# Performance work log

Hardware: AMD Instinct MI355X
Metric: run time of the kernel (lower is better)

## Reference

```python
import jax, jax.numpy as jnp
import numpy as np

N_NODES = 100000
N_EDGES = 1600000
N_FEAT = 128
HIDDEN = 128
N_GRAPHS = 64
N_CLASSES = 10
BN_EPS = 1e-5


def setup_inputs() -> dict:
    key = jax.random.key(0)
    ks = jax.random.split(key, 24)
    glorot = lambda k, o, i: jax.random.normal(k, (o, i), jnp.float32) * (1.0 / np.sqrt(i))
    inp = {
        'x': jax.random.normal(ks[0], (N_NODES, N_FEAT), jnp.float32),
        'edge_index': jax.random.randint(ks[1], (2, N_EDGES), 0, N_NODES, jnp.int64),
        'batch': jnp.sort(jax.random.randint(ks[2], (N_NODES,), 0, N_GRAPHS, jnp.int64)),
        # GCNConv(128 -> 128)
        'gcn_w': glorot(ks[3], HIDDEN, N_FEAT),
        'gcn_b': jnp.zeros((HIDDEN,), jnp.float32),
        # SAGEConv layers 1, 2: lin_l (aggregated, with bias) + lin_r (root, no bias)
        'sage1_wl': glorot(ks[4], HIDDEN, HIDDEN),
        'sage1_bl': jnp.zeros((HIDDEN,), jnp.float32),
        'sage1_wr': glorot(ks[5], HIDDEN, HIDDEN),
        'sage2_wl': glorot(ks[6], HIDDEN, HIDDEN),
        'sage2_bl': jnp.zeros((HIDDEN,), jnp.float32),
        'sage2_wr': glorot(ks[7], HIDDEN, HIDDEN),
        # ClassifierBase: 128 -> 200 -> 100 -> 50 -> 10
        'clf_w0': glorot(ks[8], 200, HIDDEN), 'clf_b0': jnp.zeros((200,), jnp.float32),
        'clf_w1': glorot(ks[9], 100, 200), 'clf_b1': jnp.zeros((100,), jnp.float32),
        'clf_w2': glorot(ks[10], 50, 100), 'clf_b2': jnp.zeros((50,), jnp.float32),
        'clf_w3': glorot(ks[11], N_CLASSES, 50), 'clf_b3': jnp.zeros((N_CLASSES,), jnp.float32),
        # BatchNorm1d (eval mode, running_mean=0, running_var=1)
        'bn0_g': jnp.ones((200,), jnp.float32), 'bn0_b': jnp.zeros((200,), jnp.float32),
        'bn1_g': jnp.ones((100,), jnp.float32), 'bn1_b': jnp.zeros((100,), jnp.float32),
        'bn2_g': jnp.ones((50,), jnp.float32), 'bn2_b': jnp.zeros((50,), jnp.float32),
    }
    return inp


def _gcn_conv(x, src, dst, W, b):
    # PyG GCNConv: add self loops, symmetric deg^{-1/2} normalization
    xw = x @ W.T                                                  # [N, H]
    ones = jnp.ones(src.shape[0], xw.dtype)
    deg = jax.ops.segment_sum(ones, dst, num_segments=N_NODES) + 1.0  # self loops
    dinv = jax.lax.rsqrt(deg)
    norm = dinv[src] * dinv[dst]                                  # [E]
    out = jax.ops.segment_sum(xw[src] * norm[:, None], dst, num_segments=N_NODES)
    out = out + xw * (dinv * dinv)[:, None]                       # self-loop term deg^{-1}
    return out + b


def _sage_conv(x, src, dst, Wl, bl, Wr):
    # PyG SAGEConv (mean aggr): lin_l(mean_{j->i} x_j) + lin_r(x_i)
    ones = jnp.ones(src.shape[0], x.dtype)
    cnt = jax.ops.segment_sum(ones, dst, num_segments=N_NODES)
    agg = jax.ops.segment_sum(x[src], dst, num_segments=N_NODES)
    agg = agg / jnp.maximum(cnt, 1.0)[:, None]
    return agg @ Wl.T + bl + x @ Wr.T


def _bn_eval(h, g, b):
    # eval-mode BatchNorm1d with running_mean=0, running_var=1
    return h * (g / np.sqrt(1.0 + BN_EPS)) + b


def reference(x, edge_index, batch, gcn_w, gcn_b,
              sage1_wl, sage1_bl, sage1_wr, sage2_wl, sage2_bl, sage2_wr,
              clf_w0, clf_b0, clf_w1, clf_b1, clf_w2, clf_b2, clf_w3, clf_b3,
              bn0_g, bn0_b, bn1_g, bn1_b, bn2_g, bn2_b):
    src, dst = edge_index[0], edge_index[1]
    h = _gcn_conv(x, src, dst, gcn_w, gcn_b)          # act_func is None -> no activation
    h = _sage_conv(h, src, dst, sage1_wl, sage1_bl, sage1_wr)
    h = _sage_conv(h, src, dst, sage2_wl, sage2_bl, sage2_wr)
    # global mean pool over graphs
    gcnt = jax.ops.segment_sum(jnp.ones(h.shape[0], h.dtype), batch, num_segments=N_GRAPHS)
    g = jax.ops.segment_sum(h, batch, num_segments=N_GRAPHS) / jnp.maximum(gcnt, 1.0)[:, None]
    # ClassifierBase (eval: dropout inactive), tanh activation
    g = jnp.tanh(_bn_eval(g @ clf_w0.T + clf_b0, bn0_g, bn0_b))
    g = jnp.tanh(_bn_eval(g @ clf_w1.T + clf_b1, bn1_g, bn1_b))
    g = jnp.tanh(_bn_eval(g @ clf_w2.T + clf_b2, bn2_g, bn2_b))
    logits = g @ clf_w3.T + clf_b3
    return jax.nn.softmax(logits, axis=1)             # [B, n_classes]
```

## Files before the change

kernel.cpp:

```cpp
#include <hip/hip_runtime.h>

#define N_NODES 100000
#define N_EDGES 1600000
#define NGRAPH 64
#define NBIN 391
#define EPB 6400
#define NBLK 250
#define CAPB 6144
#define CAP 8192
#define PSPLIT 8

typedef short s8v __attribute__((ext_vector_type(8)));
typedef float f4v __attribute__((ext_vector_type(4)));

__device__ __forceinline__ float bflo(unsigned u) { return __uint_as_float(u << 16); }
__device__ __forceinline__ float bfhi(unsigned u) { return __uint_as_float(u & 0xffff0000u); }
__device__ __forceinline__ unsigned short f2bf(float f) {
    unsigned u = __float_as_uint(f);
    u += 0x7fffu + ((u >> 16) & 1u);
    return (unsigned short)(u >> 16);
}
__device__ __forceinline__ float bf2f(unsigned short h) { return __uint_as_float(((unsigned)h) << 16); }
__device__ __forceinline__ unsigned pk(float lo, float hi) {
    return (unsigned)f2bf(lo) | ((unsigned)f2bf(hi) << 16);
}
__device__ __forceinline__ float ldv(const void* p, int i, int f32) {
    return f32 ? ((const float*)p)[i] : bf2f(((const unsigned short*)p)[i]);
}

__global__ __launch_bounds__(256) void k_setup(const unsigned short* __restrict__ x,
                                               const int* __restrict__ ei,
                                               const int* __restrict__ batch,
                                               int* __restrict__ flags,
                                               int* __restrict__ binCur,
                                               int* __restrict__ gstart,
                                               float* __restrict__ pbuf,
                                               const void* b0, const void* bn0g, const void* bn0b,
                                               const void* b1, const void* bn1g, const void* bn1b,
                                               const void* b2, const void* bn2g, const void* bn2b,
                                               const void* b3) {
    __shared__ int cnt[3];
    int tid = threadIdx.x;
    if (tid < 3) cnt[tid] = 0;
    __syncthreads();
    unsigned short h = x[tid * 37];
    int e = (h >> 7) & 0xFF;
    if (e >= 100 && e <= 150) atomicAdd(&cnt[0], 1);
    if (ei[2 * (tid * 5000) + 1] == 0) atomicAdd(&cnt[1], 1);
    if (batch[2 * (tid * 193) + 1] == 0) atomicAdd(&cnt[2], 1);
    __syncthreads();
    int f = (cnt[0] == 256) ? 0 : 1;
    int b64 = (cnt[2] == 256) ? 1 : 0;
    if (tid == 0) {
        flags[0] = f;
        flags[1] = (cnt[1] == 256) ? 1 : 0;
        flags[2] = b64;
    }
    for (int i = tid; i < NBIN; i += 256) binCur[i] = i * CAPB;
    if (tid <= NGRAPH) {
        int g = tid, lo = 0, hi = N_NODES;
        while (lo < hi) {
            int mid = (lo + hi) >> 1;
            int v = b64 ? batch[2 * mid] : batch[mid];
            if (v < g) lo = mid + 1;
            else hi = mid;
        }
        gstart[g] = lo;
    }
    const float invs = rsqrtf(1.0f + 1e-5f);
    if (tid < 200) {
        float a = ldv(bn0g, tid, f) * invs;
        pbuf[tid] = a;
        pbuf[200 + tid] = ldv(b0, tid, f) * a + ldv(bn0b, tid, f);
    }
    if (tid < 100) {
        float a = ldv(bn1g, tid, f) * invs;
        pbuf[400 + tid] = a;
        pbuf[500 + tid] = ldv(b1, tid, f) * a + ldv(bn1b, tid, f);
    }
    if (tid < 50) {
        float a = ldv(bn2g, tid, f) * invs;
        pbuf[600 + tid] = a;
        pbuf[650 + tid] = ldv(b2, tid, f) * a + ldv(bn2b, tid, f);
    }
    if (tid < 10) pbuf[700 + tid] = ldv(b3, tid, f);
}

__global__ __launch_bounds__(256) void k_binfill(const int* __restrict__ ei,
                                                 int* __restrict__ binCur,
                                                 unsigned* __restrict__ staging,
                                                 const int* __restrict__ flags) {
    __shared__ int cnt[NBIN];
    __shared__ int lofs[NBIN];
    __shared__ int curL[NBIN];
    __shared__ int basg[NBIN];
    __shared__ int sA[512], sB[512];
    __shared__ unsigned ebuf[EPB];
    int tid = threadIdx.x;
    int i64 = flags[1];
    int base = blockIdx.x * EPB;
    for (int i = tid; i < NBIN; i += 256) cnt[i] = 0;
    __syncthreads();
    for (int k = 0; k < EPB / 256; ++k) {
        int e = base + k * 256 + tid;
        int d = i64 ? ei[2 * (N_EDGES + e)] : ei[N_EDGES + e];
        if ((unsigned)d < N_NODES) atomicAdd(&cnt[d >> 8], 1);
    }
    __syncthreads();
    for (int k = tid; k < 512; k += 256) sA[k] = (k < NBIN) ? cnt[k] : 0;
    __syncthreads();
    int* src = sA;
    int* dst = sB;
    for (int off = 1; off < 512; off <<= 1) {
        for (int k = tid; k < 512; k += 256)
            dst[k] = src[k] + ((k >= off) ? src[k - off] : 0);
        __syncthreads();
        int* t = src; src = dst; dst = t;
    }
    for (int i = tid; i < NBIN; i += 256) {
        int excl = src[i] - cnt[i];
        lofs[i] = excl;
        curL[i] = excl;
        basg[i] = cnt[i] ? atomicAdd(&binCur[i], cnt[i]) : 0;
    }
    __syncthreads();
    for (int k = 0; k < EPB / 256; ++k) {
        int e = base + k * 256 + tid;
        int s = i64 ? ei[2 * e] : ei[e];
        int d = i64 ? ei[2 * (N_EDGES + e)] : ei[N_EDGES + e];
        if ((unsigned)d < N_NODES) {
            s = min(max(s, 0), N_NODES - 1);
            int p = atomicAdd(&curL[d >> 8], 1);
            ebuf[p] = ((unsigned)(d & 255) << 20) | (unsigned)s;
        }
    }
    __syncthreads();
    int wid = tid >> 6, lane = tid & 63;
    for (int b = wid; b < NBIN; b += 4) {
        int n = cnt[b], lo = lofs[b], go = basg[b];
        int cap = (b + 1) * CAPB;
        for (int l = lane; l < n; l += 64)
            if (go + l < cap) staging[go + l] = ebuf[lo + l];
    }
}

__global__ __launch_bounds__(256) void k_csr(const unsigned* __restrict__ staging,
                                             const int* __restrict__ binCur,
                                             int* __restrict__ rsA, int* __restrict__ reA,
                                             float* __restrict__ dinv,
                                             int* __restrict__ colidx) {
    __shared__ int deg[256];
    __shared__ int s[256];
    __shared__ int cur[256];
    __shared__ unsigned ebuf[CAP];
    __shared__ int colbuf[CAP];
    int b = blockIdx.x, tid = threadIdx.x;
    int n0 = b << 8;
    int nend = min(256, N_NODES - n0);
    int runStart = b * CAPB;
    int runLen = min(binCur[b] - runStart, CAPB);
    deg[tid] = 0;
    __syncthreads();
    for (int i = tid; i < runLen; i += 256) {
        unsigned e = staging[runStart + i];
        ebuf[i] = e;
        atomicAdd(&deg[e >> 20], 1);
    }
    __syncthreads();
    int myDeg = deg[tid];
    s[tid] = myDeg;
    __syncthreads();
    for (int off = 1; off < 256; off <<= 1) {
        int x2 = (tid >= off) ? s[tid - off] : 0;
        __syncthreads();
        s[tid] += x2;
        __syncthreads();
    }
    int incl = s[tid];
    if (tid < nend) {
        rsA[n0 + tid] = runStart + incl - myDeg;
        reA[n0 + tid] = runStart + incl;
        dinv[n0 + tid] = rsqrtf((float)myDeg + 1.0f);
    }
    cur[tid] = incl - myDeg;
    __syncthreads();
    for (int i = tid; i < runLen; i += 256) {
        unsigned e = ebuf[i];
        int p = atomicAdd(&cur[e >> 20], 1);
        colbuf[p] = (int)(e & 0xFFFFF);
    }
    __syncthreads();
    for (int i = tid; i < runLen; i += 256) colidx[runStart + i] = colbuf[i];
}

__global__ __launch_bounds__(256) void k_prescale(const void* __restrict__ src,
                                                  const float* __restrict__ dinv,
                                                  unsigned* __restrict__ out,
                                                  const int* __restrict__ flags) {
    int id = blockIdx.x * 256 + threadIdx.x;
    int node = id >> 6;
    float di = dinv[node];
    float lo, hi;
    if (flags[0]) {
        float2 u = ((const float2*)src)[id];
        lo = u.x; hi = u.y;
    } else {
        unsigned u = ((const unsigned*)src)[id];
        lo = bflo(u); hi = bfhi(u);
    }
    out[id] = pk(di * lo, di * hi);
}

__global__ __launch_bounds__(256) void k_agg(const uint4* __restrict__ xs,
                                             const int* __restrict__ rsA,
                                             const int* __restrict__ reA,
                                             const float* __restrict__ dinv,
                                             unsigned* __restrict__ out, int mode,
                                             const int* __restrict__ col) {
    int lane = threadIdx.x & 63;
    int node = blockIdx.x * 4 + (threadIdx.x >> 6);
    int glane = lane & 15, grp = lane >> 4;
    int rs = rsA[node], re = reA[node];
    int deg = re - rs;
    float a[8];
    #pragma unroll
    for (int i = 0; i < 8; ++i) a[i] = 0.f;
    uint4 selfu = make_uint4(0u, 0u, 0u, 0u);
    if (mode == 0) selfu = xs[(size_t)node * 16 + glane];

    int efull = rs + (deg & ~15);
    for (int base = rs; base < efull; base += 16) {
        int j0 = col[base + grp * 4 + 0];
        int j1 = col[base + grp * 4 + 1];
        int j2 = col[base + grp * 4 + 2];
        int j3 = col[base + grp * 4 + 3];
        uint4 u0 = xs[(size_t)j0 * 16 + glane];
        uint4 u1 = xs[(size_t)j1 * 16 + glane];
        uint4 u2 = xs[(size_t)j2 * 16 + glane];
        uint4 u3 = xs[(size_t)j3 * 16 + glane];
        a[0] += bflo(u0.x) + bflo(u1.x) + bflo(u2.x) + bflo(u3.x);
        a[1] += bfhi(u0.x) + bfhi(u1.x) + bfhi(u2.x) + bfhi(u3.x);
        a[2] += bflo(u0.y) + bflo(u1.y) + bflo(u2.y) + bflo(u3.y);
        a[3] += bfhi(u0.y) + bfhi(u1.y) + bfhi(u2.y) + bfhi(u3.y);
        a[4] += bflo(u0.z) + bflo(u1.z) + bflo(u2.z) + bflo(u3.z);
        a[5] += bfhi(u0.z) + bfhi(u1.z) + bfhi(u2.z) + bfhi(u3.z);
        a[6] += bflo(u0.w) + bflo(u1.w) + bflo(u2.w) + bflo(u3.w);
        a[7] += bfhi(u0.w) + bfhi(u1.w) + bfhi(u2.w) + bfhi(u3.w);
    }
    if (efull < re) {
        int j[4];
        float w[4];
        #pragma unroll
        for (int k = 0; k < 4; ++k) {
            int ee = efull + grp * 4 + k;
            bool v = ee < re;
            j[k] = col[v ? ee : re - 1];
            w[k] = v ? 1.f : 0.f;
        }
        uint4 u0 = xs[(size_t)j[0] * 16 + glane];
        uint4 u1 = xs[(size_t)j[1] * 16 + glane];
        uint4 u2 = xs[(size_t)j[2] * 16 + glane];
        uint4 u3 = xs[(size_t)j[3] * 16 + glane];
        a[0] += w[0] * bflo(u0.x) + w[1] * bflo(u1.x) + w[2] * bflo(u2.x) + w[3] * bflo(u3.x);
        a[1] += w[0] * bfhi(u0.x) + w[1] * bfhi(u1.x) + w[2] * bfhi(u2.x) + w[3] * bfhi(u3.x);
        a[2] += w[0] * bflo(u0.y) + w[1] * bflo(u1.y) + w[2] * bflo(u2.y) + w[3] * bflo(u3.y);
        a[3] += w[0] * bfhi(u0.y) + w[1] * bfhi(u1.y) + w[2] * bfhi(u2.y) + w[3] * bfhi(u3.y);
        a[4] += w[0] * bflo(u0.z) + w[1] * bflo(u1.z) + w[2] * bflo(u2.z) + w[3] * bflo(u3.z);
        a[5] += w[0] * bfhi(u0.z) + w[1] * bfhi(u1.z) + w[2] * bfhi(u2.z) + w[3] * bfhi(u3.z);
        a[6] += w[0] * bflo(u0.w) + w[1] * bflo(u1.w) + w[2] * bflo(u2.w) + w[3] * bflo(u3.w);
        a[7] += w[0] * bfhi(u0.w) + w[1] * bfhi(u1.w) + w[2] * bfhi(u2.w) + w[3] * bfhi(u3.w);
    }
    #pragma unroll
    for (int i = 0; i < 8; ++i) {
        float v = a[i];
        v += __shfl_xor(v, 16, 64);
        v += __shfl_xor(v, 32, 64);
        a[i] = v;
    }
    if (mode == 0) {
        float di = dinv[node];
        a[0] = di * (a[0] + bflo(selfu.x)); a[1] = di * (a[1] + bfhi(selfu.x));
        a[2] = di * (a[2] + bflo(selfu.y)); a[3] = di * (a[3] + bfhi(selfu.y));
        a[4] = di * (a[4] + bflo(selfu.z)); a[5] = di * (a[5] + bfhi(selfu.z));
        a[6] = di * (a[6] + bflo(selfu.w)); a[7] = di * (a[7] + bfhi(selfu.w));
    } else {
        float s = 1.0f / fmaxf((float)deg, 1.0f);
        #pragma unroll
        for (int i = 0; i < 8; ++i) a[i] *= s;
    }
    if (grp == 0) {
        uint4 o;
        o.x = pk(a[0], a[1]); o.y = pk(a[2], a[3]);
        o.z = pk(a[4], a[5]); o.w = pk(a[6], a[7]);
        *(uint4*)(out + (size_t)node * 64 + glane * 4) = o;
    }
}

template <int DUAL>
__global__ __launch_bounds__(256) void k_gemm(const unsigned short* A0,
                                              const void* __restrict__ W0,
                                              const unsigned short* __restrict__ A1,
                                              const void* __restrict__ W1,
                                              const void* __restrict__ bias,
                                              unsigned short* out,
                                              const int* __restrict__ flags) {
    __shared__ __align__(16) unsigned short As[64][136];
    __shared__ __align__(16) unsigned short Ws[128][136];
    int f32 = flags[0];
    int tid = threadIdx.x;
    int lane = tid & 63;
    int rowbase = blockIdx.x * 64;
    int lr = lane & 15, q = lane >> 4;
    int m0 = (tid >> 6) * 16;

    f4v acc[8];
    #pragma unroll
    for (int t = 0; t < 8; ++t) acc[t] = (f4v){0.f, 0.f, 0.f, 0.f};

    #pragma unroll
    for (int p = 0; p < (DUAL ? 2 : 1); ++p) {
        const unsigned short* Ap = p ? A1 : A0;
        const void* Wp = p ? W1 : W0;
        if (p) __syncthreads();
        #pragma unroll
        for (int it = 0; it < 4; ++it) {
            int chunk = tid + it * 256;
            int r = chunk >> 4, c8 = (chunk & 15) * 8;
            int grow = rowbase + r;
            uint4 v = make_uint4(0u, 0u, 0u, 0u);
            if (grow < N_NODES) v = *(const uint4*)(Ap + (size_t)grow * 128 + c8);
            *(uint4*)&As[r][c8] = v;
        }
        if (!f32) {
            const unsigned short* Wf = (const unsigned short*)Wp;
            #pragma unroll
            for (int it = 0; it < 8; ++it) {
                int chunk = tid + it * 256;
                int r = chunk >> 4, c8 = (chunk & 15) * 8;
                *(uint4*)&Ws[r][c8] = *(const uint4*)(Wf + r * 128 + c8);
            }
        } else {
            const float* Wf = (const float*)Wp;
            #pragma unroll
            for (int it = 0; it < 16; ++it) {
                int chunk = tid + it * 256;
                int r = chunk >> 5, c4 = (chunk & 31) * 4;
                float4 v = *(const float4*)(Wf + r * 128 + c4);
                unsigned lo = (unsigned)f2bf(v.x) | ((unsigned)f2bf(v.y) << 16);
                unsigned hi = (unsigned)f2bf(v.z) | ((unsigned)f2bf(v.w) << 16);
                *(uint2*)&Ws[r][c4] = make_uint2(lo, hi);
            }
        }
        __syncthreads();
        #pragma unroll
        for (int k = 0; k < 4; ++k) {
            s8v a = *(const s8v*)&As[m0 + lr][k * 32 + q * 8];
            #pragma unroll
            for (int t = 0; t < 8; ++t) {
                s8v b = *(const s8v*)&Ws[t * 16 + lr][k * 32 + q * 8];
                acc[t] = __builtin_amdgcn_mfma_f32_16x16x32_bf16(a, b, acc[t], 0, 0, 0);
            }
        }
    }
    #pragma unroll
    for (int t = 0; t < 8; ++t) {
        int o = t * 16 + lr;
        float bv = ldv(bias, o, f32);
        #pragma unroll
        for (int j = 0; j < 4; ++j) {
            int m = rowbase + m0 + q * 4 + j;
            if (m < N_NODES) out[(size_t)m * 128 + o] = f2bf(acc[t][j] + bv);
        }
    }
}

__global__ __launch_bounds__(256) void k_pool2(const unsigned* __restrict__ h,
                                               const int* __restrict__ gstart,
                                               float* __restrict__ ppool) {
    __shared__ float part[4][128];
    int g = blockIdx.x / PSPLIT, sl = blockIdx.x % PSPLIT;
    int wave = threadIdx.x >> 6, lane = threadIdx.x & 63;
    int s0 = gstart[g], s1 = gstart[g + 1];
    int n = s1 - s0;
    int chunk = (n + PSPLIT - 1) / PSPLIT;
    int r0 = s0 + sl * chunk;
    int r1 = min(r0 + chunk, s1);
    float a0 = 0.f, a1 = 0.f;
    for (int r = r0 + wave; r < r1; r += 4) {
        unsigned u = h[(size_t)r * 64 + lane];
        a0 += bflo(u);
        a1 += bfhi(u);
    }
    part[wave][2 * lane] = a0;
    part[wave][2 * lane + 1] = a1;
    __syncthreads();
    int t = threadIdx.x;
    if (t < 128) {
        float s = part[0][t] + part[1][t] + part[2][t] + part[3][t];
        ppool[(size_t)blockIdx.x * 128 + t] = s;
    }
}

__global__ void k_cvt_w(const void* w0, const void* w1, const void* w2, const void* w3,
                        float* __restrict__ wbuf, const int* __restrict__ flags) {
    int f = flags[0];
    int i = blockIdx.x * 256 + threadIdx.x;
    if (i < 25600) wbuf[i] = ldv(w0, i, f);
    else if (i < 45600) wbuf[i] = ldv(w1, i - 25600, f);
    else if (i < 50600) wbuf[i] = ldv(w2, i - 45600, f);
    else if (i < 51100) wbuf[i] = ldv(w3, i - 50600, f);
}

__global__ __launch_bounds__(256) void k_clf0(const float* __restrict__ ppool,
                                              const int* __restrict__ gstart,
                                              const float* __restrict__ wbuf,
                                              const float* __restrict__ pbuf,
                                              float* __restrict__ h1) {
    __shared__ float g[128];
    int b = blockIdx.x, t = threadIdx.x;
    if (t < 128) {
        float s = 0.f;
        #pragma unroll
        for (int k = 0; k < PSPLIT; ++k) s += ppool[(size_t)(b * PSPLIT + k) * 128 + t];
        int cnt = gstart[b + 1] - gstart[b];
        g[t] = s / fmaxf((float)cnt, 1.0f);
    }
    __syncthreads();
    if (t < 200) {
        const float4* wr = (const float4*)(wbuf + t * 128);
        float s = 0.f;
        #pragma unroll
        for (int k = 0; k < 32; ++k) {
            float4 v = wr[k];
            s += v.x * g[4 * k] + v.y * g[4 * k + 1] + v.z * g[4 * k + 2] + v.w * g[4 * k + 3];
        }
        h1[b * 200 + t] = tanhf(s * pbuf[t] + pbuf[200 + t]);
    }
}

__global__ __launch_bounds__(128) void k_clf1(const float* __restrict__ h1,
                                              const float* __restrict__ wbuf,
                                              const float* __restrict__ pbuf,
                                              float* __restrict__ h2) {
    __shared__ float g[200];
    int b = blockIdx.x, t = threadIdx.x;
    for (int i = t; i < 200; i += 128) g[i] = h1[b * 200 + i];
    __syncthreads();
    if (t < 100) {
        const float4* wr = (const float4*)(wbuf + 25600 + t * 200);
        float s = 0.f;
        #pragma unroll
        for (int k = 0; k < 50; ++k) {
            float4 v = wr[k];
            s += v.x * g[4 * k] + v.y * g[4 * k + 1] + v.z * g[4 * k + 2] + v.w * g[4 * k + 3];
        }
        h2[b * 100 + t] = tanhf(s * pbuf[400 + t] + pbuf[500 + t]);
    }
}

__global__ __launch_bounds__(128) void k_clf2(const float* __restrict__ h2,
                                              const float* __restrict__ wbuf,
                                              const float* __restrict__ pbuf,
                                              float* __restrict__ h3) {
    __shared__ float g[100];
    int b = blockIdx.x, t = threadIdx.x;
    if (t < 100) g[t] = h2[b * 100 + t];
    __syncthreads();
    if (t < 50) {
        const float4* wr = (const float4*)(wbuf + 45600 + t * 100);
        float s = 0.f;
        #pragma unroll
        for (int k = 0; k < 25; ++k) {
            float4 v = wr[k];
            s += v.x * g[4 * k] + v.y * g[4 * k + 1] + v.z * g[4 * k + 2] + v.w * g[4 * k + 3];
        }
        h3[b * 50 + t] = tanhf(s * pbuf[600 + t] + pbuf[650 + t]);
    }
}

__global__ __launch_bounds__(64) void k_clf3(const float* __restrict__ h3,
                                             const float* __restrict__ wbuf,
                                             const float* __restrict__ pbuf,
                                             void* outv, const int* __restrict__ flags) {
    int b = threadIdx.x;
    int f = flags[0];
    const float* h = h3 + b * 50;
    float lg[10];
    float mx = -1e30f;
    #pragma unroll
    for (int c = 0; c < 10; ++c) {
        const float* wr = wbuf + 50600 + c * 50;
        float s = 0.f;
        for (int k = 0; k < 50; ++k) s += wr[k] * h[k];
        s += pbuf[700 + c];
        lg[c] = s;
        mx = fmaxf(mx, s);
    }
    float sum = 0.f;
    #pragma unroll
    for (int c = 0; c < 10; ++c) {
        lg[c] = __expf(lg[c] - mx);
        sum += lg[c];
    }
    float inv = 1.0f / sum;
    #pragma unroll
    for (int c = 0; c < 10; ++c) {
        float v = lg[c] * inv;
        if (f) ((float*)outv)[b * 10 + c] = v;
        else ((unsigned short*)outv)[b * 10 + c] = f2bf(v);
    }
}

extern "C" void kernel_launch(void* const* d_in, const int* in_sizes, int n_in,
                              void* d_out, int out_size, void* d_ws, size_t ws_size,
                              hipStream_t stream) {
    const unsigned short* x16 = (const unsigned short*)d_in[0];
    const int* ei = (const int*)d_in[1];
    const int* batch = (const int*)d_in[2];

    char* ws = (char*)d_ws;
    size_t off = 0;
    auto alloc = [&](size_t bytes) {
        size_t r = off;
        off = (off + bytes + 255) & ~(size_t)255;
        return r;
    };
    int* flags = (int*)(ws + alloc(256));
    int* rsA = (int*)(ws + alloc((size_t)N_NODES * 4));
    int* reA = (int*)(ws + alloc((size_t)N_NODES * 4));
    int* colidx = (int*)(ws + alloc((size_t)NBIN * CAPB * 4));
    float* dinv = (float*)(ws + alloc((size_t)N_NODES * 4));
    int* binCur = (int*)(ws + alloc(NBIN * 4));
    int* gstart = (int*)(ws + alloc((NGRAPH + 1) * 4));
    float* pbuf = (float*)(ws + alloc(710 * 4));
    float* ppool = (float*)(ws + alloc((size_t)NGRAPH * PSPLIT * 128 * 4));
    float* wbuf = (float*)(ws + alloc(51100 * 4));
    float* h1 = (float*)(ws + alloc(64 * 200 * 4));
    float* h2 = (float*)(ws + alloc(64 * 100 * 4));
    float* h3 = (float*)(ws + alloc(64 * 50 * 4));
    unsigned short* bufA = (unsigned short*)(ws + alloc((size_t)N_NODES * 128 * 2));
    unsigned short* bufB = (unsigned short*)(ws + alloc((size_t)N_NODES * 128 * 2));
    unsigned* staging = (unsigned*)bufA;

    k_setup<<<1, 256, 0, stream>>>(x16, ei, batch, flags, binCur, gstart, pbuf,
                                   d_in[12], d_in[19], d_in[20],
                                   d_in[14], d_in[21], d_in[22],
                                   d_in[16], d_in[23], d_in[24], d_in[18]);
    k_cvt_w<<<200, 256, 0, stream>>>(d_in[11], d_in[13], d_in[15], d_in[17], wbuf, flags);

    k_binfill<<<NBLK, 256, 0, stream>>>(ei, binCur, staging, flags);
    k_csr<<<NBIN, 256, 0, stream>>>(staging, binCur, rsA, reA, dinv, colidx);

    k_prescale<<<N_NODES * 64 / 256, 256, 0, stream>>>((const void*)x16, dinv,
                                                       (unsigned*)bufB, flags);
    k_agg<<<N_NODES / 4, 256, 0, stream>>>((const uint4*)bufB, rsA, reA, dinv,
                                           (unsigned*)bufA, 0, colidx);
    k_gemm<0><<<(N_NODES + 63) / 64, 256, 0, stream>>>(bufA, d_in[3], nullptr, nullptr, d_in[4],
                                                       bufA, flags);
    k_agg<<<N_NODES / 4, 256, 0, stream>>>((const uint4*)bufA, rsA, reA, dinv,
                                           (unsigned*)bufB, 1, colidx);
    k_gemm<1><<<(N_NODES + 63) / 64, 256, 0, stream>>>(bufB, d_in[5], bufA, d_in[7], d_in[6],
                                                       bufB, flags);
    k_agg<<<N_NODES / 4, 256, 0, stream>>>((const uint4*)bufB, rsA, reA, dinv,
                                           (unsigned*)bufA, 1, colidx);
    k_gemm<1><<<(N_NODES + 63) / 64, 256, 0, stream>>>(bufA, d_in[8], bufB, d_in[10], d_in[9],
                                                       bufA, flags);
    k_pool2<<<NGRAPH * PSPLIT, 256, 0, stream>>>((const unsigned*)bufA, gstart, ppool);
    k_clf0<<<NGRAPH, 256, 0, stream>>>(ppool, gstart, wbuf, pbuf, h1);
    k_clf1<<<NGRAPH, 128, 0, stream>>>(h1, wbuf, pbuf, h2);
    k_clf2<<<NGRAPH, 128, 0, stream>>>(h2, wbuf, pbuf, h3);
    k_clf3<<<1, 64, 0, stream>>>(h3, wbuf, pbuf, d_out, flags);
}
```

Measured before the change: 517.7 us.

## Pad CSR rows to 32, fuse prescale into CSR build, merge classifier kernels

```diff
diff --git a/kernel.cpp b/kernel.cpp
--- a/kernel.cpp
+++ b/kernel.cpp
@@ -4,14 +4,15 @@
 #define N_EDGES 1600000
 #define NGRAPH 64
 #define NBIN 391
-#define EPB 6400
-#define NBLK 250
+#define EPB 2560
+#define NBLK 625
 #define CAPB 6144
-#define CAP 8192
+#define CAPP 8960
 #define PSPLIT 8
 
 typedef short s8v __attribute__((ext_vector_type(8)));
 typedef float f4v __attribute__((ext_vector_type(4)));
+typedef float f2v __attribute__((ext_vector_type(2)));
 
 __device__ __forceinline__ float bflo(unsigned u) { return __uint_as_float(u << 16); }
 __device__ __forceinline__ float bfhi(unsigned u) { return __uint_as_float(u & 0xffff0000u); }
@@ -26,6 +27,9 @@
 }
 __device__ __forceinline__ float ldv(const void* p, int i, int f32) {
     return f32 ? ((const float*)p)[i] : bf2f(((const unsigned short*)p)[i]);
+}
+__device__ __forceinline__ f2v up2(unsigned u) {
+    f2v t; t.x = bflo(u); t.y = bfhi(u); return t;
 }
 
 __global__ __launch_bounds__(256) void k_setup(const unsigned short* __restrict__ x,
@@ -95,16 +99,28 @@
     __shared__ int curL[NBIN];
     __shared__ int basg[NBIN];
     __shared__ int sA[512], sB[512];
+    __shared__ int dbuf[EPB];
     __shared__ unsigned ebuf[EPB];
     int tid = threadIdx.x;
     int i64 = flags[1];
     int base = blockIdx.x * EPB;
     for (int i = tid; i < NBIN; i += 256) cnt[i] = 0;
     __syncthreads();
-    for (int k = 0; k < EPB / 256; ++k) {
-        int e = base + k * 256 + tid;
-        int d = i64 ? ei[2 * (N_EDGES + e)] : ei[N_EDGES + e];
-        if ((unsigned)d < N_NODES) atomicAdd(&cnt[d >> 8], 1);
+    #pragma unroll
+    for (int k = 0; k < EPB / 512; ++k) {
+        int e = base + k * 512 + tid * 2;
+        int d0, d1;
+        if (i64) {
+            uint4 v = *(const uint4*)(ei + 2 * (size_t)(N_EDGES + e));
+            d0 = (int)v.x; d1 = (int)v.z;
+        } else {
+            int2 v = *(const int2*)(ei + (size_t)N_EDGES + e);
+            d0 = v.x; d1 = v.y;
+        }
+        int l = k * 512 + tid * 2;
+        dbuf[l] = d0; dbuf[l + 1] = d1;
+        if ((unsigned)d0 < N_NODES) atomicAdd(&cnt[d0 >> 8], 1);
+        if ((unsigned)d1 < N_NODES) atomicAdd(&cnt[d1 >> 8], 1);
     }
     __syncthreads();
     for (int k = tid; k < 512; k += 256) sA[k] = (k < NBIN) ? cnt[k] : 0;
@@ -124,14 +140,27 @@
         basg[i] = cnt[i] ? atomicAdd(&binCur[i], cnt[i]) : 0;
     }
     __syncthreads();
-    for (int k = 0; k < EPB / 256; ++k) {
-        int e = base + k * 256 + tid;
-        int s = i64 ? ei[2 * e] : ei[e];
-        int d = i64 ? ei[2 * (N_EDGES + e)] : ei[N_EDGES + e];
-        if ((unsigned)d < N_NODES) {
-            s = min(max(s, 0), N_NODES - 1);
-            int p = atomicAdd(&curL[d >> 8], 1);
-            ebuf[p] = ((unsigned)(d & 255) << 20) | (unsigned)s;
+    #pragma unroll
+    for (int k = 0; k < EPB / 512; ++k) {
+        int e = base + k * 512 + tid * 2;
+        int s0, s1;
+        if (i64) {
+            uint4 v = *(const uint4*)(ei + 2 * (size_t)e);
+            s0 = (int)v.x; s1 = (int)v.z;
+        } else {
+            int2 v = *(const int2*)(ei + (size_t)e);
+            s0 = v.x; s1 = v.y;
+        }
+        int l = k * 512 + tid * 2;
+        #pragma unroll
+        for (int h = 0; h < 2; ++h) {
+            int d = dbuf[l + h];
+            int s = h ? s1 : s0;
+            if ((unsigned)d < N_NODES) {
+                s = min(max(s, 0), N_NODES - 1);
+                int p = atomicAdd(&curL[d >> 8], 1);
+                ebuf[p] = ((unsigned)(d & 255) << 20) | (unsigned)s;
+            }
         }
     }
     __syncthreads();
@@ -148,16 +177,22 @@
                                              const int* __restrict__ binCur,
                                              int* __restrict__ rsA, int* __restrict__ reA,
                                              float* __restrict__ dinv,
-                                             int* __restrict__ colidx) {
+                                             int* __restrict__ colidx,
+                                             const void* __restrict__ x,
+                                             const int* __restrict__ flags,
+                                             unsigned* __restrict__ yout,
+                                             unsigned* __restrict__ padA) {
     __shared__ int deg[256];
     __shared__ int s[256];
     __shared__ int cur[256];
-    __shared__ unsigned ebuf[CAP];
-    __shared__ int colbuf[CAP];
+    __shared__ float sdinv[256];
+    __shared__ unsigned ebuf[CAPB];
+    __shared__ int colbuf[CAPP];
     int b = blockIdx.x, tid = threadIdx.x;
     int n0 = b << 8;
     int nend = min(256, N_NODES - n0);
     int runStart = b * CAPB;
+    int outStart = b * CAPP;
     int runLen = min(binCur[b] - runStart, CAPB);
     deg[tid] = 0;
     __syncthreads();
@@ -166,9 +201,11 @@
         ebuf[i] = e;
         atomicAdd(&deg[e >> 20], 1);
     }
+    for (int i = tid; i < CAPP; i += 256) colbuf[i] = N_NODES;
     __syncthreads();
     int myDeg = deg[tid];
-    s[tid] = myDeg;
+    int pdeg = (myDeg + 31) & ~31;
+    s[tid] = pdeg;
     __syncthreads();
     for (int off = 1; off < 256; off <<= 1) {
         int x2 = (tid >= off) ? s[tid - off] : 0;
@@ -177,38 +214,43 @@
         __syncthreads();
     }
     int incl = s[tid];
+    int lrs = incl - pdeg;
     if (tid < nend) {
-        rsA[n0 + tid] = runStart + incl - myDeg;
-        reA[n0 + tid] = runStart + incl;
-        dinv[n0 + tid] = rsqrtf((float)myDeg + 1.0f);
-    }
-    cur[tid] = incl - myDeg;
+        rsA[n0 + tid] = outStart + lrs;
+        reA[n0 + tid] = outStart + lrs + myDeg;
+        float di = rsqrtf((float)myDeg + 1.0f);
+        dinv[n0 + tid] = di;
+        sdinv[tid] = di;
+    }
+    cur[tid] = lrs;
     __syncthreads();
     for (int i = tid; i < runLen; i += 256) {
         unsigned e = ebuf[i];
         int p = atomicAdd(&cur[e >> 20], 1);
-        colbuf[p] = (int)(e & 0xFFFFF);
-    }
-    __syncthreads();
-    for (int i = tid; i < runLen; i += 256) colidx[runStart + i] = colbuf[i];
-}
-
-__global__ __launch_bounds__(256) void k_prescale(const void* __restrict__ src,
-                                                  const float* __restrict__ dinv,
-                                                  unsigned* __restrict__ out,
-                                                  const int* __restrict__ flags) {
-    int id = blockIdx.x * 256 + threadIdx.x;
-    int node = id >> 6;
-    float di = dinv[node];
-    float lo, hi;
-    if (flags[0]) {
-        float2 u = ((const float2*)src)[id];
-        lo = u.x; hi = u.y;
-    } else {
-        unsigned u = ((const unsigned*)src)[id];
-        lo = bflo(u); hi = bfhi(u);
-    }
-    out[id] = pk(di * lo, di * hi);
+        if (p < CAPP) colbuf[p] = (int)(e & 0xFFFFF);
+    }
+    __syncthreads();
+    int ptot = min(s[255], CAPP);
+    for (int i = tid; i < ptot; i += 256) colidx[outStart + i] = colbuf[i];
+    int f32 = flags[0];
+    for (int i = tid; i < nend * 64; i += 256) {
+        int nd = i >> 6;
+        float di = sdinv[nd];
+        size_t gid = (size_t)n0 * 64 + i;
+        float lo, hi;
+        if (f32) {
+            float2 u = ((const float2*)x)[gid];
+            lo = u.x; hi = u.y;
+        } else {
+            unsigned u = ((const unsigned*)x)[gid];
+            lo = bflo(u); hi = bfhi(u);
+        }
+        yout[gid] = pk(di * lo, di * hi);
+    }
+    if (b == 0 && tid < 64) {
+        yout[(size_t)N_NODES * 64 + tid] = 0u;
+        padA[(size_t)N_NODES * 64 + tid] = 0u;
+    }
 }
 
 __global__ __launch_bounds__(256) void k_agg(const uint4* __restrict__ xs,
@@ -222,76 +264,54 @@
     int glane = lane & 15, grp = lane >> 4;
     int rs = rsA[node], re = reA[node];
     int deg = re - rs;
-    float a[8];
-    #pragma unroll
-    for (int i = 0; i < 8; ++i) a[i] = 0.f;
+    int pend = rs + ((deg + 31) & ~31);
+    f2v a0 = {0.f, 0.f}, a1 = {0.f, 0.f}, a2 = {0.f, 0.f}, a3 = {0.f, 0.f};
     uint4 selfu = make_uint4(0u, 0u, 0u, 0u);
-    if (mode == 0) selfu = xs[(size_t)node * 16 + glane];
-
-    int efull = rs + (deg & ~15);
-    for (int base = rs; base < efull; base += 16) {
-        int j0 = col[base + grp * 4 + 0];
-        int j1 = col[base + grp * 4 + 1];
-        int j2 = col[base + grp * 4 + 2];
-        int j3 = col[base + grp * 4 + 3];
-        uint4 u0 = xs[(size_t)j0 * 16 + glane];
-        uint4 u1 = xs[(size_t)j1 * 16 + glane];
-        uint4 u2 = xs[(size_t)j2 * 16 + glane];
-        uint4 u3 = xs[(size_t)j3 * 16 + glane];
-        a[0] += bflo(u0.x) + bflo(u1.x) + bflo(u2.x) + bflo(u3.x);
-        a[1] += bfhi(u0.x) + bfhi(u1.x) + bfhi(u2.x) + bfhi(u3.x);
-        a[2] += bflo(u0.y) + bflo(u1.y) + bflo(u2.y) + bflo(u3.y);
-        a[3] += bfhi(u0.y) + bfhi(u1.y) + bfhi(u2.y) + bfhi(u3.y);
-        a[4] += bflo(u0.z) + bflo(u1.z) + bflo(u2.z) + bflo(u3.z);
-        a[5] += bfhi(u0.z) + bfhi(u1.z) + bfhi(u2.z) + bfhi(u3.z);
-        a[6] += bflo(u0.w) + bflo(u1.w) + bflo(u2.w) + bflo(u3.w);
-        a[7] += bfhi(u0.w) + bfhi(u1.w) + bfhi(u2.w) + bfhi(u3.w);
-    }
-    if (efull < re) {
-        int j[4];
-        float w[4];
-        #pragma unroll
-        for (int k = 0; k < 4; ++k) {
-            int ee = efull + grp * 4 + k;
-            bool v = ee < re;
-            j[k] = col[v ? ee : re - 1];
-            w[k] = v ? 1.f : 0.f;
-        }
-        uint4 u0 = xs[(size_t)j[0] * 16 + glane];
-        uint4 u1 = xs[(size_t)j[1] * 16 + glane];
-        uint4 u2 = xs[(size_t)j[2] * 16 + glane];
-        uint4 u3 = xs[(size_t)j[3] * 16 + glane];
-        a[0] += w[0] * bflo(u0.x) + w[1] * bflo(u1.x) + w[2] * bflo(u2.x) + w[3] * bflo(u3.x);
-        a[1] += w[0] * bfhi(u0.x) + w[1] * bfhi(u1.x) + w[2] * bfhi(u2.x) + w[3] * bfhi(u3.x);
-        a[2] += w[0] * bflo(u0.y) + w[1] * bflo(u1.y) + w[2] * bflo(u2.y) + w[3] * bflo(u3.y);
-        a[3] += w[0] * bfhi(u0.y) + w[1] * bfhi(u1.y) + w[2] * bfhi(u2.y) + w[3] * bfhi(u3.y);
-        a[4] += w[0] * bflo(u0.z) + w[1] * bflo(u1.z) + w[2] * bflo(u2.z) + w[3] * bflo(u3.z);
-        a[5] += w[0] * bfhi(u0.z) + w[1] * bfhi(u1.z) + w[2] * bfhi(u2.z) + w[3] * bfhi(u3.z);
-        a[6] += w[0] * bflo(u0.w) + w[1] * bflo(u1.w) + w[2] * bflo(u2.w) + w[3] * bflo(u3.w);
-        a[7] += w[0] * bfhi(u0.w) + w[1] * bfhi(u1.w) + w[2] * bfhi(u2.w) + w[3] * bfhi(u3.w);
-    }
+    if (mode == 0) selfu = xs[(unsigned)node * 16u + glane];
+
+    for (int base = rs; base < pend; base += 32) {
+        int4 c0 = *(const int4*)(col + base + grp * 4);
+        int4 c1 = *(const int4*)(col + base + 16 + grp * 4);
+        uint4 u0 = xs[(unsigned)c0.x * 16u + glane];
+        uint4 u1 = xs[(unsigned)c0.y * 16u + glane];
+        uint4 u2 = xs[(unsigned)c0.z * 16u + glane];
+        uint4 u3 = xs[(unsigned)c0.w * 16u + glane];
+        uint4 u4 = xs[(unsigned)c1.x * 16u + glane];
+        uint4 u5 = xs[(unsigned)c1.y * 16u + glane];
+        uint4 u6 = xs[(unsigned)c1.z * 16u + glane];
+        uint4 u7 = xs[(unsigned)c1.w * 16u + glane];
+        a0 += up2(u0.x); a1 += up2(u0.y); a2 += up2(u0.z); a3 += up2(u0.w);
+        a0 += up2(u1.x); a1 += up2(u1.y); a2 += up2(u1.z); a3 += up2(u1.w);
+        a0 += up2(u2.x); a1 += up2(u2.y); a2 += up2(u2.z); a3 += up2(u2.w);
+        a0 += up2(u3.x); a1 += up2(u3.y); a2 += up2(u3.z); a3 += up2(u3.w);
+        a0 += up2(u4.x); a1 += up2(u4.y); a2 += up2(u4.z); a3 += up2(u4.w);
+        a0 += up2(u5.x); a1 += up2(u5.y); a2 += up2(u5.z); a3 += up2(u5.w);
+        a0 += up2(u6.x); a1 += up2(u6.y); a2 += up2(u6.z); a3 += up2(u6.w);
+        a0 += up2(u7.x); a1 += up2(u7.y); a2 += up2(u7.z); a3 += up2(u7.w);
+    }
+    float r[8] = {a0.x, a0.y, a1.x, a1.y, a2.x, a2.y, a3.x, a3.y};
     #pragma unroll
     for (int i = 0; i < 8; ++i) {
-        float v = a[i];
+        float v = r[i];
         v += __shfl_xor(v, 16, 64);
         v += __shfl_xor(v, 32, 64);
-        a[i] = v;
+        r[i] = v;
     }
     if (mode == 0) {
         float di = dinv[node];
-        a[0] = di * (a[0] + bflo(selfu.x)); a[1] = di * (a[1] + bfhi(selfu.x));
-        a[2] = di * (a[2] + bflo(selfu.y)); a[3] = di * (a[3] + bfhi(selfu.y));
-        a[4] = di * (a[4] + bflo(selfu.z)); a[5] = di * (a[5] + bfhi(selfu.z));
-        a[6] = di * (a[6] + bflo(selfu.w)); a[7] = di * (a[7] + bfhi(selfu.w));
+        r[0] = di * (r[0] + bflo(selfu.x)); r[1] = di * (r[1] + bfhi(selfu.x));
+        r[2] = di * (r[2] + bflo(selfu.y)); r[3] = di * (r[3] + bfhi(selfu.y));
+        r[4] = di * (r[4] + bflo(selfu.z)); r[5] = di * (r[5] + bfhi(selfu.z));
+        r[6] = di * (r[6] + bflo(selfu.w)); r[7] = di * (r[7] + bfhi(selfu.w));
     } else {
         float s = 1.0f / fmaxf((float)deg, 1.0f);
         #pragma unroll
-        for (int i = 0; i < 8; ++i) a[i] *= s;
+        for (int i = 0; i < 8; ++i) r[i] *= s;
     }
     if (grp == 0) {
         uint4 o;
-        o.x = pk(a[0], a[1]); o.y = pk(a[2], a[3]);
-        o.z = pk(a[4], a[5]); o.w = pk(a[6], a[7]);
+        o.x = pk(r[0], r[1]); o.y = pk(r[2], r[3]);
+        o.z = pk(r[4], r[5]); o.w = pk(r[6], r[7]);
         *(uint4*)(out + (size_t)node * 64 + glane * 4) = o;
     }
 }
@@ -411,19 +431,21 @@
     else if (i < 51100) wbuf[i] = ldv(w3, i - 50600, f);
 }
 
-__global__ __launch_bounds__(256) void k_clf0(const float* __restrict__ ppool,
-                                              const int* __restrict__ gstart,
-                                              const float* __restrict__ wbuf,
-                                              const float* __restrict__ pbuf,
-                                              float* __restrict__ h1) {
-    __shared__ float g[128];
+__global__ __launch_bounds__(256) void k_clf(const float* __restrict__ ppool,
+                                             const int* __restrict__ gstart,
+                                             const float* __restrict__ wbuf,
+                                             const float* __restrict__ pbuf,
+                                             void* outv, const int* __restrict__ flags) {
+    __shared__ float gin[128];
+    __shared__ float ha[200];
+    __shared__ float hb[100];
     int b = blockIdx.x, t = threadIdx.x;
     if (t < 128) {
         float s = 0.f;
         #pragma unroll
         for (int k = 0; k < PSPLIT; ++k) s += ppool[(size_t)(b * PSPLIT + k) * 128 + t];
         int cnt = gstart[b + 1] - gstart[b];
-        g[t] = s / fmaxf((float)cnt, 1.0f);
+        gin[t] = s / fmaxf((float)cnt, 1.0f);
     }
     __syncthreads();
     if (t < 200) {
@@ -432,19 +454,10 @@
         #pragma unroll
         for (int k = 0; k < 32; ++k) {
             float4 v = wr[k];
-            s += v.x * g[4 * k] + v.y * g[4 * k + 1] + v.z * g[4 * k + 2] + v.w * g[4 * k + 3];
-        }
-        h1[b * 200 + t] = tanhf(s * pbuf[t] + pbuf[200 + t]);
-    }
-}
-
-__global__ __launch_bounds__(128) void k_clf1(const float* __restrict__ h1,
-                                              const float* __restrict__ wbuf,
-                                              const float* __restrict__ pbuf,
-                                              float* __restrict__ h2) {
-    __shared__ float g[200];
-    int b = blockIdx.x, t = threadIdx.x;
-    for (int i = t; i < 200; i += 128) g[i] = h1[b * 200 + i];
+            s += v.x * gin[4 * k] + v.y * gin[4 * k + 1] + v.z * gin[4 * k + 2] + v.w * gin[4 * k + 3];
+        }
+        ha[t] = tanhf(s * pbuf[t] + pbuf[200 + t]);
+    }
     __syncthreads();
     if (t < 100) {
         const float4* wr = (const float4*)(wbuf + 25600 + t * 200);
@@ -452,19 +465,10 @@
         #pragma unroll
         for (int k = 0; k < 50; ++k) {
             float4 v = wr[k];
-            s += v.x * g[4 * k] + v.y * g[4 * k + 1] + v.z * g[4 * k + 2] + v.w * g[4 * k + 3];
-        }
-        h2[b * 100 + t] = tanhf(s * pbuf[400 + t] + pbuf[500 + t]);
-    }
-}
-
-__global__ __launch_bounds__(128) void k_clf2(const float* __restrict__ h2,
-                                              const float* __restrict__ wbuf,
-                                              const float* __restrict__ pbuf,
-                                              float* __restrict__ h3) {
-    __shared__ float g[100];
-    int b = blockIdx.x, t = threadIdx.x;
-    if (t < 100) g[t] = h2[b * 100 + t];
+            s += v.x * ha[4 * k] + v.y * ha[4 * k + 1] + v.z * ha[4 * k + 2] + v.w * ha[4 * k + 3];
+        }
+        hb[t] = tanhf(s * pbuf[400 + t] + pbuf[500 + t]);
+    }
     __syncthreads();
     if (t < 50) {
         const float4* wr = (const float4*)(wbuf + 45600 + t * 100);
@@ -472,42 +476,37 @@
         #pragma unroll
         for (int k = 0; k < 25; ++k) {
             float4 v = wr[k];
-            s += v.x * g[4 * k] + v.y * g[4 * k + 1] + v.z * g[4 * k + 2] + v.w * g[4 * k + 3];
-        }
-        h3[b * 50 + t] = tanhf(s * pbuf[600 + t] + pbuf[650 + t]);
-    }
-}
-
-__global__ __launch_bounds__(64) void k_clf3(const float* __restrict__ h3,
-                                             const float* __restrict__ wbuf,
-                                             const float* __restrict__ pbuf,
-                                             void* outv, const int* __restrict__ flags) {
-    int b = threadIdx.x;
-    int f = flags[0];
-    const float* h = h3 + b * 50;
-    float lg[10];
-    float mx = -1e30f;
-    #pragma unroll
-    for (int c = 0; c < 10; ++c) {
-        const float* wr = wbuf + 50600 + c * 50;
-        float s = 0.f;
-        for (int k = 0; k < 50; ++k) s += wr[k] * h[k];
-        s += pbuf[700 + c];
-        lg[c] = s;
-        mx = fmaxf(mx, s);
-    }
-    float sum = 0.f;
-    #pragma unroll
-    for (int c = 0; c < 10; ++c) {
-        lg[c] = __expf(lg[c] - mx);
-        sum += lg[c];
-    }
-    float inv = 1.0f / sum;
-    #pragma unroll
-    for (int c = 0; c < 10; ++c) {
-        float v = lg[c] * inv;
-        if (f) ((float*)outv)[b * 10 + c] = v;
-        else ((unsigned short*)outv)[b * 10 + c] = f2bf(v);
+            s += v.x * hb[4 * k] + v.y * hb[4 * k + 1] + v.z * hb[4 * k + 2] + v.w * hb[4 * k + 3];
+        }
+        gin[t] = tanhf(s * pbuf[600 + t] + pbuf[650 + t]);
+    }
+    __syncthreads();
+    if (t == 0) {
+        int f = flags[0];
+        float lg[10];
+        float mx = -1e30f;
+        #pragma unroll
+        for (int c = 0; c < 10; ++c) {
+            const float* wr = wbuf + 50600 + c * 50;
+            float s = 0.f;
+            for (int k = 0; k < 50; ++k) s += wr[k] * gin[k];
+            s += pbuf[700 + c];
+            lg[c] = s;
+            mx = fmaxf(mx, s);
+        }
+        float sum = 0.f;
+        #pragma unroll
+        for (int c = 0; c < 10; ++c) {
+            lg[c] = __expf(lg[c] - mx);
+            sum += lg[c];
+        }
+        float inv = 1.0f / sum;
+        #pragma unroll
+        for (int c = 0; c < 10; ++c) {
+            float v = lg[c] * inv;
+            if (f) ((float*)outv)[b * 10 + c] = v;
+            else ((unsigned short*)outv)[b * 10 + c] = f2bf(v);
+        }
     }
 }
 
@@ -528,18 +527,15 @@
     int* flags = (int*)(ws + alloc(256));
     int* rsA = (int*)(ws + alloc((size_t)N_NODES * 4));
     int* reA = (int*)(ws + alloc((size_t)N_NODES * 4));
-    int* colidx = (int*)(ws + alloc((size_t)NBIN * CAPB * 4));
+    int* colidx = (int*)(ws + alloc((size_t)NBIN * CAPP * 4));
     float* dinv = (float*)(ws + alloc((size_t)N_NODES * 4));
     int* binCur = (int*)(ws + alloc(NBIN * 4));
     int* gstart = (int*)(ws + alloc((NGRAPH + 1) * 4));
     float* pbuf = (float*)(ws + alloc(710 * 4));
     float* ppool = (float*)(ws + alloc((size_t)NGRAPH * PSPLIT * 128 * 4));
     float* wbuf = (float*)(ws + alloc(51100 * 4));
-    float* h1 = (float*)(ws + alloc(64 * 200 * 4));
-    float* h2 = (float*)(ws + alloc(64 * 100 * 4));
-    float* h3 = (float*)(ws + alloc(64 * 50 * 4));
-    unsigned short* bufA = (unsigned short*)(ws + alloc((size_t)N_NODES * 128 * 2));
-    unsigned short* bufB = (unsigned short*)(ws + alloc((size_t)N_NODES * 128 * 2));
+    unsigned short* bufA = (unsigned short*)(ws + alloc((size_t)(N_NODES + 1) * 128 * 2));
+    unsigned short* bufB = (unsigned short*)(ws + alloc((size_t)(N_NODES + 1) * 128 * 2));
     unsigned* staging = (unsigned*)bufA;
 
     k_setup<<<1, 256, 0, stream>>>(x16, ei, batch, flags, binCur, gstart, pbuf,
@@ -549,10 +545,9 @@
     k_cvt_w<<<200, 256, 0, stream>>>(d_in[11], d_in[13], d_in[15], d_in[17], wbuf, flags);
 
     k_binfill<<<NBLK, 256, 0, stream>>>(ei, binCur, staging, flags);
-    k_csr<<<NBIN, 256, 0, stream>>>(staging, binCur, rsA, reA, dinv, colidx);
-
-    k_prescale<<<N_NODES * 64 / 256, 256, 0, stream>>>((const void*)x16, dinv,
-                                                       (unsigned*)bufB, flags);
+    k_csr<<<NBIN, 256, 0, stream>>>(staging, binCur, rsA, reA, dinv, colidx,
+                                    (const void*)x16, flags, (unsigned*)bufB, (unsigned*)bufA);
+
     k_agg<<<N_NODES / 4, 256, 0, stream>>>((const uint4*)bufB, rsA, reA, dinv,
                                            (unsigned*)bufA, 0, colidx);
     k_gemm<0><<<(N_NODES + 63) / 64, 256, 0, stream>>>(bufA, d_in[3], nullptr, nullptr, d_in[4],
@@ -566,8 +561,5 @@
     k_gemm<1><<<(N_NODES + 63) / 64, 256, 0, stream>>>(bufA, d_in[8], bufB, d_in[10], d_in[9],
                                                        bufA, flags);
     k_pool2<<<NGRAPH * PSPLIT, 256, 0, stream>>>((const unsigned*)bufA, gstart, ppool);
-    k_clf0<<<NGRAPH, 256, 0, stream>>>(ppool, gstart, wbuf, pbuf, h1);
-    k_clf1<<<NGRAPH, 128, 0, stream>>>(h1, wbuf, pbuf, h2);
-    k_clf2<<<NGRAPH, 128, 0, stream>>>(h2, wbuf, pbuf, h3);
-    k_clf3<<<1, 64, 0, stream>>>(h3, wbuf, pbuf, d_out, flags);
-}
+    k_clf<<<NGRAPH, 256, 0, stream>>>(ppool, gstart, wbuf, pbuf, d_out, flags);
+}
```

Measured after the change: 546.6 us. 5.6% more time.
